# Kernel tuning notes

Hardware: AMD Instinct MI355X
Metric: run time of the kernel (lower is better)

Reference implementation:

```python
import jax, jax.numpy as jnp
import numpy as np

BN_EPS = 1e-5


def setup_inputs() -> dict:
    key = jax.random.key(0)
    ks = jax.random.split(key, 12)
    B, N, S, D1, D2 = 8, 8192, 2048, 128, 256
    C_in = D2 + D1  # 384
    mlp = [256, 128]
    inp = {
        "xyz1": jax.random.normal(ks[0], (B, 3, N), jnp.float32),
        "xyz2": jax.random.normal(ks[1], (B, 3, S), jnp.float32),
        "points1": jax.random.normal(ks[2], (B, D1, N), jnp.float32),
        "points2": jax.random.normal(ks[3], (B, D2, S), jnp.float32),
    }
    # conv0: in 384 -> 256, conv1: 256 -> 128 (1x1 Conv1d == per-point matmul)
    inp["w0"] = jax.random.normal(ks[4], (mlp[0], C_in), jnp.float32) * (1.0 / np.sqrt(C_in))
    inp["b0"] = jax.random.normal(ks[5], (mlp[0],), jnp.float32) * 0.01
    inp["g0"] = jnp.ones((mlp[0],), jnp.float32)
    inp["be0"] = jnp.zeros((mlp[0],), jnp.float32)
    inp["w1"] = jax.random.normal(ks[6], (mlp[1], mlp[0]), jnp.float32) * (1.0 / np.sqrt(mlp[0]))
    inp["b1"] = jax.random.normal(ks[7], (mlp[1],), jnp.float32) * 0.01
    inp["g1"] = jnp.ones((mlp[1],), jnp.float32)
    inp["be1"] = jnp.zeros((mlp[1],), jnp.float32)
    return inp


def _conv_bn_relu(x, w, b, g, be):
    # 1x1 Conv1d + BatchNorm1d (training-mode batch stats, biased var) + ReLU
    x = jnp.einsum("oc,bcn->bon", w, x) + b[None, :, None]
    m = jnp.mean(x, axis=(0, 2), keepdims=True)
    v = jnp.var(x, axis=(0, 2), keepdims=True)
    x = (x - m) * jax.lax.rsqrt(v + BN_EPS) * g[None, :, None] + be[None, :, None]
    return jax.nn.relu(x)


def reference(xyz1, xyz2, points1, points2, w0, b0, g0, be0, w1, b1, g1, be1):
    B, _, N = xyz1.shape
    S = xyz2.shape[2]
    src = jnp.transpose(xyz1, (0, 2, 1))  # [B,N,3]
    dst = jnp.transpose(xyz2, (0, 2, 1))  # [B,S,3]
    # squared pairwise distance [B,N,S]
    dist = (
        jnp.sum(src * src, axis=-1)[:, :, None]
        + jnp.sum(dst * dst, axis=-1)[:, None, :]
        - 2.0 * jnp.einsum("bnc,bsc->bns", src, dst)
    )
    # 3 nearest neighbors (smallest dist, sorted)
    neg_d, idx = jax.lax.top_k(-dist, 3)  # [B,N,3]
    d3 = -neg_d
    recip = 1.0 / (d3 + 1e-8)
    weight = recip / jnp.sum(recip, axis=-1, keepdims=True)  # [B,N,3]
    p2t = jnp.transpose(points2, (0, 2, 1))  # [B,S,D']
    gathered = jnp.take_along_axis(
        p2t, idx.reshape(B, N * 3)[:, :, None], axis=1
    ).reshape(B, N, 3, -1)  # [B,N,3,D']
    interp = jnp.einsum("bnkd,bnk->bdn", gathered, weight)  # [B,D',N]
    x = jnp.concatenate([interp, points1], axis=1)  # [B,D'+D,N]
    x = _conv_bn_relu(x, w0, b0, g0, be0)
    x = _conv_bn_relu(x, w1, b1, g1, be1)
    return x
```

## Files before the change

### kernel.cpp

```cpp
#include <hip/hip_runtime.h>
#include <hip/hip_bf16.h>

constexpr int kB = 8, kN = 8192, kS = 2048;
constexpr int kD1 = 128, kD2 = 256, kCin = 384, kM0 = 256, kM1 = 128;
constexpr float kEps = 1e-5f;

typedef float f32x4 __attribute__((ext_vector_type(4)));
typedef short bf16x8 __attribute__((ext_vector_type(8)));
typedef unsigned short u16x4 __attribute__((ext_vector_type(4)));

__device__ inline unsigned short f2bf(float f) {
    __hip_bfloat16 h = __float2bfloat16(f);
    return *reinterpret_cast<unsigned short*>(&h);
}
__device__ inline float bf2f(unsigned short u) {
    unsigned int v = (unsigned int)u << 16;
    return *reinterpret_cast<float*>(&v);
}
__device__ inline unsigned uminu(unsigned a, unsigned b) { return a < b ? a : b; }
__device__ inline unsigned med3u(unsigned a, unsigned b, unsigned c) {
    unsigned d;
    asm("v_med3_u32 %0, %1, %2, %3" : "=v"(d) : "v"(a), "v"(b), "v"(c));
    return d;
}
#define INS4(K0, K1, K2, K3, X) do { unsigned _x = (X);          \
    K3 = med3u(_x, K2, K3);                                      \
    K2 = med3u(_x, K1, K2);                                      \
    K1 = med3u(_x, K0, K1);                                      \
    K0 = uminu(_x, K0); } while (0)

__global__ __launch_bounds__(256) void prep_kernel(
    const float* __restrict__ points2, float* __restrict__ p2t,
    const float* __restrict__ points1, unsigned short* __restrict__ xt,
    const float* __restrict__ xyz2, f32x4* __restrict__ spk, float* __restrict__ stats)
{
    __shared__ float tl[64][69];
    const int bx = blockIdx.x;
    const int t = threadIdx.x;
    const int rlo = t >> 4, rhi = t & 15;
    if (bx < 1024) {
        const int b = bx >> 7, tile = bx & 127;
        const int s0 = (tile & 31) * 64, c0 = (tile >> 5) * 64;
#pragma unroll
        for (int r = 0; r < 4; ++r) {
            const int cl = rlo + r * 16;
            f32x4 v = *(const f32x4*)(points2 + ((size_t)(b * kD2 + c0 + cl)) * kS + s0 + rhi * 4);
#pragma unroll
            for (int j = 0; j < 4; ++j) tl[cl][rhi * 4 + j] = v[j];
        }
        __syncthreads();
#pragma unroll
        for (int r = 0; r < 4; ++r) {
            const int sl = rlo + r * 16;
            f32x4 v;
#pragma unroll
            for (int j = 0; j < 4; ++j) v[j] = tl[rhi * 4 + j][sl];
            *(f32x4*)(p2t + ((size_t)(b * kS + s0 + sl)) * kD2 + c0 + rhi * 4) = v;
        }
    } else if (bx < 3072) {
        const int idx = bx - 1024;
        const int b = idx >> 8, tile = idx & 255;
        const int n0 = (tile & 127) * 64, c0 = (tile >> 7) * 64;
#pragma unroll
        for (int r = 0; r < 4; ++r) {
            const int cl = rlo + r * 16;
            f32x4 v = *(const f32x4*)(points1 + ((size_t)(b * kD1 + c0 + cl)) * kN + n0 + rhi * 4);
#pragma unroll
            for (int j = 0; j < 4; ++j) tl[cl][rhi * 4 + j] = v[j];
        }
        __syncthreads();
#pragma unroll
        for (int r = 0; r < 4; ++r) {
            const int nl = rlo + r * 16;
            u16x4 u;
#pragma unroll
            for (int j = 0; j < 4; ++j) u[j] = f2bf(tl[rhi * 4 + j][nl]);
            *(u16x4*)(xt + ((size_t)(b * kN + n0 + nl)) * kCin + 256 + c0 + rhi * 4) = u;
        }
    } else {
        const int b = bx - 3072;
        const float* x2 = xyz2 + b * 3 * kS;
        for (int s = t; s < kS; s += 256) {
            float sx = x2[s], sy = x2[kS + s], sz = x2[2 * kS + s];
            f32x4 q = {sx, sy, sz, fmaf(sx, sx, fmaf(sy, sy, sz * sz))};
            spk[b * kS + s] = q;
        }
        if (b == 0) for (int i = t; i < 1792; i += 256) stats[i] = 0.f;
    }
}

__global__ __launch_bounds__(256) void knn_interp_kernel(
    const float* __restrict__ xyz1, const f32x4* __restrict__ spk,
    const float* __restrict__ p2t, unsigned short* __restrict__ xt,
    int* __restrict__ flaglist, int* __restrict__ flagcount)
{
    __shared__ f32x4 sp[kS];
    const int bb = blockIdx.x >> 7;
    const int nblk = (blockIdx.x & 127) << 6;
    const int t = threadIdx.x;
    for (int s = t; s < kS; s += 256) sp[s] = spk[bb * kS + s];
    __syncthreads();
    const int q = t >> 2, c = t & 3;
    const int nq = nblk + q;
    const float* x1 = xyz1 + bb * 3 * kN;
    const float px = x1[nq], py = x1[kN + nq], pz = x1[2 * kN + nq];
    const float ax = -2.f * px, ay = -2.f * py, az = -2.f * pz;
    const float pp = fmaf(px, px, fmaf(py, py, pz * pz));

    unsigned k0 = 0xFFFFFFFFu, k1 = 0xFFFFFFFFu, k2 = 0xFFFFFFFFu, k3 = 0xFFFFFFFFu;
#pragma unroll 8
    for (int i = 0; i < 512; ++i) {
        const f32x4 qv = sp[4 * i + c];
        const float e = fmaxf(fmaf(ax, qv[0], fmaf(ay, qv[1], fmaf(az, qv[2], qv[3] + pp))), 0.f);
        const unsigned x = (__float_as_uint(e) & 0xFFFFF800u) | (unsigned)(4 * i + c);
        INS4(k0, k1, k2, k3, x);
    }
#pragma unroll
    for (int off = 1; off <= 2; off <<= 1) {
        const unsigned m0 = __shfl_xor(k0, off), m1 = __shfl_xor(k1, off);
        const unsigned m2 = __shfl_xor(k2, off), m3 = __shfl_xor(k3, off);
        INS4(k0, k1, k2, k3, m0); INS4(k0, k1, k2, k3, m1);
        INS4(k0, k1, k2, k3, m2); INS4(k0, k1, k2, k3, m3);
    }

    bool flag = false;
    float w0f = 0.f, w1f = 0.f, w2f = 0.f;
    int i0 = (int)(k0 & 2047u), i1 = (int)(k1 & 2047u), i2 = (int)(k2 & 2047u);
    if (c == 0) {
        const float v2t = __uint_as_float(k2 & 0xFFFFF800u);
        const float v3t = __uint_as_float(k3 & 0xFFFFF800u);
        flag = (v3t - v2t) <= fmaf(v3t, 1e-3f, 2.5e-4f);
        const double dpx = (double)px, dpy = (double)py, dpz = (double)pz;
        const f32x4 s0 = sp[i0], s1 = sp[i1], s2 = sp[i2];
        double d0 = (dpx - s0[0]) * (dpx - s0[0]) + (dpy - s0[1]) * (dpy - s0[1]) + (dpz - s0[2]) * (dpz - s0[2]);
        double d1 = (dpx - s1[0]) * (dpx - s1[0]) + (dpy - s1[1]) * (dpy - s1[1]) + (dpz - s1[2]) * (dpz - s1[2]);
        double d2 = (dpx - s2[0]) * (dpx - s2[0]) + (dpy - s2[1]) * (dpy - s2[1]) + (dpz - s2[2]) * (dpz - s2[2]);
        if (d1 < d0 || (d1 == d0 && i1 < i0)) { double td = d0; d0 = d1; d1 = td; int ti = i0; i0 = i1; i1 = ti; }
        if (d2 < d1 || (d2 == d1 && i2 < i1)) { double td = d1; d1 = d2; d2 = td; int ti = i1; i1 = i2; i2 = ti; }
        if (d1 < d0 || (d1 == d0 && i1 < i0)) { double td = d0; d0 = d1; d1 = td; int ti = i0; i0 = i1; i1 = ti; }
        const double r0 = 1.0 / (d0 + 1e-8), r1 = 1.0 / (d1 + 1e-8), r2 = 1.0 / (d2 + 1e-8);
        const double rs = 1.0 / (r0 + r1 + r2);
        w0f = (float)(r0 * rs); w1f = (float)(r1 * rs); w2f = (float)(r2 * rs);
    }
    const int src = (t & 63) & ~3;
    w0f = __shfl(w0f, src); w1f = __shfl(w1f, src); w2f = __shfl(w2f, src);
    i0 = __shfl(i0, src); i1 = __shfl(i1, src); i2 = __shfl(i2, src);

    {
        const unsigned long long bal = __ballot(flag);
        if (bal) {
            const int l = t & 63;
            int base = 0;
            if (l == 0) base = atomicAdd(flagcount, __popcll(bal));
            base = __shfl(base, 0);
            if (flag) {
                const int pre = __popcll(bal & ((1ull << l) - 1ull));
                flaglist[base + pre] = (bb << 13) | nq;
            }
        }
    }

    const f32x4* row0 = (const f32x4*)(p2t + ((size_t)(bb * kS) + i0) * kD2);
    const f32x4* row1 = (const f32x4*)(p2t + ((size_t)(bb * kS) + i1) * kD2);
    const f32x4* row2 = (const f32x4*)(p2t + ((size_t)(bb * kS) + i2) * kD2);
    unsigned short* dst = xt + ((size_t)(bb * kN) + nq) * kCin;
#pragma unroll 4
    for (int j = 0; j < 16; ++j) {
        const int ch = c + 4 * j;
        f32x4 v = w0f * row0[ch] + w1f * row1[ch] + w2f * row2[ch];
        u16x4 u = {f2bf(v[0]), f2bf(v[1]), f2bf(v[2]), f2bf(v[3])};
        *(u16x4*)(dst + ch * 4) = u;
    }
}
#undef INS4

__global__ __launch_bounds__(256) void knn_fallback_kernel(
    const float* __restrict__ xyz1, const f32x4* __restrict__ spk,
    const float* __restrict__ p2t, unsigned short* __restrict__ xt,
    const int* __restrict__ flaglist, const int* __restrict__ flagcount)
{
    const int cnt = *flagcount;
    const int t = threadIdx.x;
    const int w = t >> 6, l = t & 63;
    for (int idx = blockIdx.x * 4 + w; idx < cnt; idx += gridDim.x * 4) {
        const int code = flaglist[idx];
        const int b = code >> 13, n = code & 8191;
        const float* x1 = xyz1 + b * 3 * kN;
        const double px = (double)x1[n], py = (double)x1[kN + n], pz = (double)x1[2 * kN + n];
        double d0 = 1e300, d1 = 1e300, d2 = 1e300;
        int i0 = 0, i1 = 0, i2 = 0;
        for (int s = l; s < kS; s += 64) {
            const f32x4 q = spk[b * kS + s];
            const double ex = px - (double)q[0], ey = py - (double)q[1], ez = pz - (double)q[2];
            const double d = ex * ex + ey * ey + ez * ez;
            if (d < d2) {
                if (d < d1) {
                    if (d < d0) { d2 = d1; i2 = i1; d1 = d0; i1 = i0; d0 = d; i0 = s; }
                    else        { d2 = d1; i2 = i1; d1 = d;  i1 = s; }
                } else          { d2 = d;  i2 = s; }
            }
        }
#pragma unroll
        for (int off = 1; off < 64; off <<= 1) {
            double pd0 = __shfl_xor(d0, off), pd1 = __shfl_xor(d1, off), pd2 = __shfl_xor(d2, off);
            int pi0 = __shfl_xor(i0, off), pi1 = __shfl_xor(i1, off), pi2 = __shfl_xor(i2, off);
#pragma unroll
            for (int m = 0; m < 3; ++m) {
                const double pd = (m == 0) ? pd0 : (m == 1) ? pd1 : pd2;
                const int pi = (m == 0) ? pi0 : (m == 1) ? pi1 : pi2;
                if (pd < d2 || (pd == d2 && pi < i2)) {
                    if (pd < d1 || (pd == d1 && pi < i1)) {
                        if (pd < d0 || (pd == d0 && pi < i0)) {
                            d2 = d1; i2 = i1; d1 = d0; i1 = i0; d0 = pd; i0 = pi;
                        } else { d2 = d1; i2 = i1; d1 = pd; i1 = pi; }
                    } else { d2 = pd; i2 = pi; }
                }
            }
        }
        const double r0 = 1.0 / (d0 + 1e-8), r1 = 1.0 / (d1 + 1e-8), r2 = 1.0 / (d2 + 1e-8);
        const double rs = 1.0 / (r0 + r1 + r2);
        const float w0f = (float)(r0 * rs), w1f = (float)(r1 * rs), w2f = (float)(r2 * rs);
        const f32x4* row0 = (const f32x4*)(p2t + ((size_t)(b * kS) + i0) * kD2);
        const f32x4* row1 = (const f32x4*)(p2t + ((size_t)(b * kS) + i1) * kD2);
        const f32x4* row2 = (const f32x4*)(p2t + ((size_t)(b * kS) + i2) * kD2);
        const f32x4 v = w0f * row0[l] + w1f * row1[l] + w2f * row2[l];
        u16x4 u = {f2bf(v[0]), f2bf(v[1]), f2bf(v[2]), f2bf(v[3])};
        *(u16x4*)(xt + ((size_t)(b * kN) + n) * kCin + l * 4) = u;
    }
}

__device__ inline int swz(int row, int ks) {
    return row * 32 + ((ks ^ ((row >> 1) & 3)) << 3);
}

template <int K, int MTOT, bool BNRELU, int OUTMODE, bool STATS>
__global__ __launch_bounds__(256) void gemm_bn_kernel(
    const float* __restrict__ W, const unsigned short* __restrict__ X,
    const float* __restrict__ bn_sum, const float* __restrict__ bn_sq,
    const float* __restrict__ bn_g, const float* __restrict__ bn_be,
    unsigned short* __restrict__ Yb, float* __restrict__ Yf,
    float* __restrict__ gsum, float* __restrict__ gsq)
{
    constexpr int BM = 128, BN = 128;
    __shared__ unsigned short Al[BM * 32], Bl[BN * 32];
    __shared__ float ssum[BM], ssq[BM];
    __shared__ float s_sc[K > 0 ? K : 1], s_sh[K > 0 ? K : 1];
    const int t = threadIdx.x;
    const int bn = blockIdx.x * BN, bo = blockIdx.y * BM, b = blockIdx.z;
    const int l = t & 63, w = t >> 6;
    const int wm = (w >> 1) * 64, wn = (w & 1) * 64;
    const int lrow = l & 15, lks = l >> 4;

    if constexpr (BNRELU) {
        if (t < K) {
            const float invn = 1.0f / 65536.0f;
            const float mean = bn_sum[t] * invn;
            const float var = bn_sq[t] * invn - mean * mean;
            const float sc = bn_g[t] * rsqrtf(var + kEps);
            s_sc[t] = sc;
            s_sh[t] = fmaf(-mean, sc, bn_be[t]);
        }
    }
    if constexpr (STATS) {
        if (t < BM) { ssum[t] = 0.f; ssq[t] = 0.f; }
    }
    __syncthreads();

    f32x4 acc[4][4] = {};
    for (int k0 = 0; k0 < K; k0 += 32) {
#pragma unroll
        for (int r = 0; r < 2; ++r) {
            const int sid = t + r * 256;
            const int m = sid >> 2, ks = sid & 3;
            const float* wp = W + (size_t)(bo + m) * K + k0 + ks * 8;
            f32x4 wa = *(const f32x4*)wp, wb = *(const f32x4*)(wp + 4);
            bf16x8 u;
#pragma unroll
            for (int j = 0; j < 4; ++j) { u[j] = (short)f2bf(wa[j]); u[j + 4] = (short)f2bf(wb[j]); }
            *(bf16x8*)(Al + swz(m, ks)) = u;
        }
#pragma unroll
        for (int r = 0; r < 2; ++r) {
            const int sid = t + r * 256;
            const int nl = sid >> 2, ks = sid & 3;
            bf16x8 v = *(const bf16x8*)(X + ((size_t)(b * kN) + bn + nl) * K + k0 + ks * 8);
            if constexpr (BNRELU) {
#pragma unroll
                for (int j = 0; j < 8; ++j) {
                    const int ch = k0 + ks * 8 + j;
                    float f = fmaxf(fmaf(bf2f((unsigned short)v[j]), s_sc[ch], s_sh[ch]), 0.f);
                    v[j] = (short)f2bf(f);
                }
            }
            *(bf16x8*)(Bl + swz(nl, ks)) = v;
        }
        __syncthreads();
        bf16x8 af[4], bfr[4];
#pragma unroll
        for (int f = 0; f < 4; ++f) af[f]  = *(const bf16x8*)(Al + swz(wm + f * 16 + lrow, lks));
#pragma unroll
        for (int f = 0; f < 4; ++f) bfr[f] = *(const bf16x8*)(Bl + swz(wn + f * 16 + lrow, lks));
#pragma unroll
        for (int mi = 0; mi < 4; ++mi)
#pragma unroll
            for (int ni = 0; ni < 4; ++ni)
                acc[mi][ni] = __builtin_amdgcn_mfma_f32_16x16x32_bf16(af[mi], bfr[ni], acc[mi][ni], 0, 0, 0);
        __syncthreads();
    }

    if constexpr (STATS) {
#pragma unroll
        for (int mi = 0; mi < 4; ++mi) {
#pragma unroll
            for (int r = 0; r < 4; ++r) {
                float ps = 0.f, pq = 0.f;
#pragma unroll
                for (int ni = 0; ni < 4; ++ni) { float v = acc[mi][ni][r]; ps += v; pq += v * v; }
#pragma unroll
                for (int off = 1; off < 16; off <<= 1) { ps += __shfl_xor(ps, off); pq += __shfl_xor(pq, off); }
                if (lrow == 0) {
                    const int m = wm + mi * 16 + lks * 4 + r;
                    atomicAdd(&ssum[m], ps); atomicAdd(&ssq[m], pq);
                }
            }
        }
    }

    if constexpr (OUTMODE == 0) {
#pragma unroll
        for (int mi = 0; mi < 4; ++mi)
#pragma unroll
            for (int ni = 0; ni < 4; ++ni) {
                const int m = bo + wm + mi * 16 + lks * 4;
                const int n = bn + wn + ni * 16 + lrow;
                u16x4 u = {f2bf(acc[mi][ni][0]), f2bf(acc[mi][ni][1]),
                           f2bf(acc[mi][ni][2]), f2bf(acc[mi][ni][3])};
                *(u16x4*)(Yb + ((size_t)(b * kN) + n) * MTOT + m) = u;
            }
    } else {
#pragma unroll
        for (int mi = 0; mi < 4; ++mi)
#pragma unroll
            for (int ni = 0; ni < 4; ++ni) {
                const int n = bn + wn + ni * 16 + lrow;
#pragma unroll
                for (int r = 0; r < 4; ++r) {
                    const int m = bo + wm + mi * 16 + lks * 4 + r;
                    Yf[((size_t)(b * MTOT) + m) * kN + n] = acc[mi][ni][r];
                }
            }
    }
    if constexpr (STATS) {
        __syncthreads();
        if (t < BM) {
            atomicAdd(&gsum[bo + t], ssum[t]);
            atomicAdd(&gsq[bo + t], ssq[t]);
        }
    }
}

__global__ __launch_bounds__(256) void bn_relu_out_kernel(
    float* __restrict__ out, const float* __restrict__ bn_sum, const float* __restrict__ bn_sq,
    const float* __restrict__ bn_g, const float* __restrict__ bn_be)
{
    __shared__ float ssc[kM1], ssh[kM1];
    const int t = threadIdx.x;
    if (t < kM1) {
        const float invn = 1.0f / 65536.0f;
        const float mean = bn_sum[t] * invn;
        const float var = bn_sq[t] * invn - mean * mean;
        const float sc = bn_g[t] * rsqrtf(var + kEps);
        ssc[t] = sc;
        ssh[t] = fmaf(-mean, sc, bn_be[t]);
    }
    __syncthreads();
    const int total = kB * kM1 * kN / 4;
    for (int idx = blockIdx.x * blockDim.x + t; idx < total; idx += gridDim.x * blockDim.x) {
        const int p = (idx >> 11) & 127;
        const float sc = ssc[p], sh = ssh[p];
        f32x4 v = ((f32x4*)out)[idx];
#pragma unroll
        for (int j = 0; j < 4; ++j) v[j] = fmaxf(fmaf(v[j], sc, sh), 0.f);
        ((f32x4*)out)[idx] = v;
    }
}

extern "C" void kernel_launch(void* const* d_in, const int* in_sizes, int n_in,
                              void* d_out, int out_size, void* d_ws, size_t ws_size,
                              hipStream_t stream)
{
    const float* xyz1    = (const float*)d_in[0];
    const float* xyz2    = (const float*)d_in[1];
    const float* points1 = (const float*)d_in[2];
    const float* points2 = (const float*)d_in[3];
    const float* w0      = (const float*)d_in[4];
    const float* g0      = (const float*)d_in[6];
    const float* be0     = (const float*)d_in[7];
    const float* w1      = (const float*)d_in[8];
    const float* g1      = (const float*)d_in[10];
    const float* be1     = (const float*)d_in[11];
    float* out = (float*)d_out;

    char* ws = (char*)d_ws;
    unsigned short* xt  = (unsigned short*)ws;
    float* p2t          = (float*)(ws + (size_t)50331648);
    unsigned short* y0t = (unsigned short*)(ws + (size_t)67108864);
    float* stats        = (float*)(ws + (size_t)100663296);
    f32x4* spk          = (f32x4*)(ws + (size_t)104857600);
    int*  flaglist      = (int*)(ws + (size_t)105906176);
    float* sum0 = stats,          *sq0 = stats + 256;
    float* sum1 = stats + 512,    *sq1 = stats + 640;
    int*  flagcount = (int*)(stats + 1536);

    prep_kernel<<<3080, 256, 0, stream>>>(points2, p2t, points1, xt, xyz2, spk, stats);
    knn_interp_kernel<<<1024, 256, 0, stream>>>(xyz1, spk, p2t, xt, flaglist, flagcount);
    knn_fallback_kernel<<<1024, 256, 0, stream>>>(xyz1, spk, p2t, xt, flaglist, flagcount);
    gemm_bn_kernel<kCin, kM0, false, 0, true><<<dim3(64, 2, 8), 256, 0, stream>>>(
        w0, xt, nullptr, nullptr, nullptr, nullptr, y0t, nullptr, sum0, sq0);
    gemm_bn_kernel<kM0, kM1, true, 1, true><<<dim3(64, 1, 8), 256, 0, stream>>>(
        w1, y0t, sum0, sq0, g0, be0, nullptr, out, sum1, sq1);
    bn_relu_out_kernel<<<2048, 256, 0, stream>>>(out, sum1, sq1, g1, be1);
}
```

Before: 167.9 us.

## Pre-convert weights to bf16, double-buffer GEMM LDS tiles, halve N tile

Weights w0/w1 are now converted to bf16 once inside the prep kernel, so each GEMM block no longer re-reads and re-converts fp32 weights every K step. The GEMM kernel gets register-staged double buffering in LDS: the next tile's global loads are issued before the current tile's MFMAs, and one sync per K step is dropped. The N tile shrinks from 128 to 64, which doubles the grid for better occupancy and load balance but lowers per-block reuse of the A tile. It also adds extra workspace buffers and a few more prep blocks.

```diff
diff --git a/kernel.cpp b/kernel.cpp
--- a/kernel.cpp
+++ b/kernel.cpp
@@ -32,7 +32,9 @@
 __global__ __launch_bounds__(256) void prep_kernel(
     const float* __restrict__ points2, float* __restrict__ p2t,
     const float* __restrict__ points1, unsigned short* __restrict__ xt,
-    const float* __restrict__ xyz2, f32x4* __restrict__ spk, float* __restrict__ stats)
+    const float* __restrict__ xyz2, f32x4* __restrict__ spk, float* __restrict__ stats,
+    const float* __restrict__ w0, unsigned short* __restrict__ w0bf,
+    const float* __restrict__ w1, unsigned short* __restrict__ w1bf)
 {
     __shared__ float tl[64][69];
     const int bx = blockIdx.x;
@@ -77,7 +79,7 @@
             for (int j = 0; j < 4; ++j) u[j] = f2bf(tl[rhi * 4 + j][nl]);
             *(u16x4*)(xt + ((size_t)(b * kN + n0 + nl)) * kCin + 256 + c0 + rhi * 4) = u;
         }
-    } else {
+    } else if (bx < 3080) {
         const int b = bx - 3072;
         const float* x2 = xyz2 + b * 3 * kS;
         for (int s = t; s < kS; s += 256) {
@@ -86,6 +88,20 @@
             spk[b * kS + s] = q;
         }
         if (b == 0) for (int i = t; i < 1792; i += 256) stats[i] = 0.f;
+    } else if (bx < 3096) {
+        const int base = (bx - 3080) * 256 + t;
+        for (int c = base; c < kM0 * kCin / 4; c += 4096) {
+            f32x4 v = *(const f32x4*)(w0 + (size_t)c * 4);
+            u16x4 u = {f2bf(v[0]), f2bf(v[1]), f2bf(v[2]), f2bf(v[3])};
+            *(u16x4*)(w0bf + (size_t)c * 4) = u;
+        }
+    } else {
+        const int base = (bx - 3096) * 256 + t;
+        for (int c = base; c < kM1 * kM0 / 4; c += 2048) {
+            f32x4 v = *(const f32x4*)(w1 + (size_t)c * 4);
+            u16x4 u = {f2bf(v[0]), f2bf(v[1]), f2bf(v[2]), f2bf(v[3])};
+            *(u16x4*)(w1bf + (size_t)c * 4) = u;
+        }
     }
 }
 
@@ -235,20 +251,20 @@
 
 template <int K, int MTOT, bool BNRELU, int OUTMODE, bool STATS>
 __global__ __launch_bounds__(256) void gemm_bn_kernel(
-    const float* __restrict__ W, const unsigned short* __restrict__ X,
+    const unsigned short* __restrict__ Wbf, const unsigned short* __restrict__ X,
     const float* __restrict__ bn_sum, const float* __restrict__ bn_sq,
     const float* __restrict__ bn_g, const float* __restrict__ bn_be,
     unsigned short* __restrict__ Yb, float* __restrict__ Yf,
     float* __restrict__ gsum, float* __restrict__ gsq)
 {
-    constexpr int BM = 128, BN = 128;
-    __shared__ unsigned short Al[BM * 32], Bl[BN * 32];
+    constexpr int BM = 128, BN = 64;
+    __shared__ unsigned short Al[2][BM * 32], Bl[2][BN * 32];
     __shared__ float ssum[BM], ssq[BM];
-    __shared__ float s_sc[K > 0 ? K : 1], s_sh[K > 0 ? K : 1];
+    __shared__ float s_sc[K], s_sh[K];
     const int t = threadIdx.x;
     const int bn = blockIdx.x * BN, bo = blockIdx.y * BM, b = blockIdx.z;
     const int l = t & 63, w = t >> 6;
-    const int wm = (w >> 1) * 64, wn = (w & 1) * 64;
+    const int wm = (w >> 1) * 64, wn = (w & 1) * 32;
     const int lrow = l & 15, lks = l >> 4;
 
     if constexpr (BNRELU) {
@@ -266,45 +282,49 @@
     }
     __syncthreads();
 
-    f32x4 acc[4][4] = {};
-    for (int k0 = 0; k0 < K; k0 += 32) {
-#pragma unroll
-        for (int r = 0; r < 2; ++r) {
-            const int sid = t + r * 256;
-            const int m = sid >> 2, ks = sid & 3;
-            const float* wp = W + (size_t)(bo + m) * K + k0 + ks * 8;
-            f32x4 wa = *(const f32x4*)wp, wb = *(const f32x4*)(wp + 4);
-            bf16x8 u;
-#pragma unroll
-            for (int j = 0; j < 4; ++j) { u[j] = (short)f2bf(wa[j]); u[j + 4] = (short)f2bf(wb[j]); }
-            *(bf16x8*)(Al + swz(m, ks)) = u;
-        }
-#pragma unroll
-        for (int r = 0; r < 2; ++r) {
-            const int sid = t + r * 256;
-            const int nl = sid >> 2, ks = sid & 3;
-            bf16x8 v = *(const bf16x8*)(X + ((size_t)(b * kN) + bn + nl) * K + k0 + ks * 8);
-            if constexpr (BNRELU) {
-#pragma unroll
-                for (int j = 0; j < 8; ++j) {
-                    const int ch = k0 + ks * 8 + j;
-                    float f = fmaxf(fmaf(bf2f((unsigned short)v[j]), s_sc[ch], s_sh[ch]), 0.f);
-                    v[j] = (short)f2bf(f);
-                }
-            }
-            *(bf16x8*)(Bl + swz(nl, ks)) = v;
-        }
-        __syncthreads();
-        bf16x8 af[4], bfr[4];
-#pragma unroll
-        for (int f = 0; f < 4; ++f) af[f]  = *(const bf16x8*)(Al + swz(wm + f * 16 + lrow, lks));
-#pragma unroll
-        for (int f = 0; f < 4; ++f) bfr[f] = *(const bf16x8*)(Bl + swz(wn + f * 16 + lrow, lks));
+    const int mA0 = t >> 2, ksA = t & 3;
+    const int mA1 = mA0 + 64;
+    const int nB = t >> 2, ksB = t & 3;
+    bf16x8 rA0, rA1, rB;
+
+    auto load_tile = [&](int k0) {
+        rA0 = *(const bf16x8*)(Wbf + (size_t)(bo + mA0) * K + k0 + ksA * 8);
+        rA1 = *(const bf16x8*)(Wbf + (size_t)(bo + mA1) * K + k0 + ksA * 8);
+        rB  = *(const bf16x8*)(X + ((size_t)(b * kN) + bn + nB) * K + k0 + ksB * 8);
+    };
+    auto write_tile = [&](int buf, int k0) {
+        *(bf16x8*)(&Al[buf][0] + swz(mA0, ksA)) = rA0;
+        *(bf16x8*)(&Al[buf][0] + swz(mA1, ksA)) = rA1;
+        bf16x8 v = rB;
+        if constexpr (BNRELU) {
+#pragma unroll
+            for (int j = 0; j < 8; ++j) {
+                const int ch = k0 + ksB * 8 + j;
+                float f = fmaxf(fmaf(bf2f((unsigned short)v[j]), s_sc[ch], s_sh[ch]), 0.f);
+                v[j] = (short)f2bf(f);
+            }
+        }
+        *(bf16x8*)(&Bl[buf][0] + swz(nB, ksB)) = v;
+    };
+
+    f32x4 acc[4][2] = {};
+    load_tile(0);
+    write_tile(0, 0);
+    __syncthreads();
+    int cur = 0;
+    for (int k0 = 32; k0 <= K; k0 += 32) {
+        if (k0 < K) load_tile(k0);
+        bf16x8 af[4], bfr[2];
+#pragma unroll
+        for (int f = 0; f < 4; ++f) af[f]  = *(const bf16x8*)(&Al[cur][0] + swz(wm + f * 16 + lrow, lks));
+#pragma unroll
+        for (int f = 0; f < 2; ++f) bfr[f] = *(const bf16x8*)(&Bl[cur][0] + swz(wn + f * 16 + lrow, lks));
 #pragma unroll
         for (int mi = 0; mi < 4; ++mi)
 #pragma unroll
-            for (int ni = 0; ni < 4; ++ni)
+            for (int ni = 0; ni < 2; ++ni)
                 acc[mi][ni] = __builtin_amdgcn_mfma_f32_16x16x32_bf16(af[mi], bfr[ni], acc[mi][ni], 0, 0, 0);
+        if (k0 < K) { write_tile(cur ^ 1, k0); cur ^= 1; }
         __syncthreads();
     }
 
@@ -315,7 +335,7 @@
             for (int r = 0; r < 4; ++r) {
                 float ps = 0.f, pq = 0.f;
 #pragma unroll
-                for (int ni = 0; ni < 4; ++ni) { float v = acc[mi][ni][r]; ps += v; pq += v * v; }
+                for (int ni = 0; ni < 2; ++ni) { float v = acc[mi][ni][r]; ps += v; pq += v * v; }
 #pragma unroll
                 for (int off = 1; off < 16; off <<= 1) { ps += __shfl_xor(ps, off); pq += __shfl_xor(pq, off); }
                 if (lrow == 0) {
@@ -330,7 +350,7 @@
 #pragma unroll
         for (int mi = 0; mi < 4; ++mi)
 #pragma unroll
-            for (int ni = 0; ni < 4; ++ni) {
+            for (int ni = 0; ni < 2; ++ni) {
                 const int m = bo + wm + mi * 16 + lks * 4;
                 const int n = bn + wn + ni * 16 + lrow;
                 u16x4 u = {f2bf(acc[mi][ni][0]), f2bf(acc[mi][ni][1]),
@@ -341,7 +361,7 @@
 #pragma unroll
         for (int mi = 0; mi < 4; ++mi)
 #pragma unroll
-            for (int ni = 0; ni < 4; ++ni) {
+            for (int ni = 0; ni < 2; ++ni) {
                 const int n = bn + wn + ni * 16 + lrow;
 #pragma unroll
                 for (int r = 0; r < 4; ++r) {
@@ -408,16 +428,19 @@
     float* stats        = (float*)(ws + (size_t)100663296);
     f32x4* spk          = (f32x4*)(ws + (size_t)104857600);
     int*  flaglist      = (int*)(ws + (size_t)105906176);
+    unsigned short* w0bf = (unsigned short*)(ws + (size_t)106954752);
+    unsigned short* w1bf = (unsigned short*)(ws + (size_t)107151360);
     float* sum0 = stats,          *sq0 = stats + 256;
     float* sum1 = stats + 512,    *sq1 = stats + 640;
     int*  flagcount = (int*)(stats + 1536);
 
-    prep_kernel<<<3080, 256, 0, stream>>>(points2, p2t, points1, xt, xyz2, spk, stats);
+    prep_kernel<<<3104, 256, 0, stream>>>(points2, p2t, points1, xt, xyz2, spk, stats,
+                                          w0, w0bf, w1, w1bf);
     knn_interp_kernel<<<1024, 256, 0, stream>>>(xyz1, spk, p2t, xt, flaglist, flagcount);
     knn_fallback_kernel<<<1024, 256, 0, stream>>>(xyz1, spk, p2t, xt, flaglist, flagcount);
-    gemm_bn_kernel<kCin, kM0, false, 0, true><<<dim3(64, 2, 8), 256, 0, stream>>>(
-        w0, xt, nullptr, nullptr, nullptr, nullptr, y0t, nullptr, sum0, sq0);
-    gemm_bn_kernel<kM0, kM1, true, 1, true><<<dim3(64, 1, 8), 256, 0, stream>>>(
-        w1, y0t, sum0, sq0, g0, be0, nullptr, out, sum1, sq1);
+    gemm_bn_kernel<kCin, kM0, false, 0, true><<<dim3(128, 2, 8), 256, 0, stream>>>(
+        w0bf, xt, nullptr, nullptr, nullptr, nullptr, y0t, nullptr, sum0, sq0);
+    gemm_bn_kernel<kM0, kM1, true, 1, true><<<dim3(128, 1, 8), 256, 0, stream>>>(
+        w1bf, y0t, sum0, sq0, g0, be0, nullptr, out, sum1, sq1);
     bn_relu_out_kernel<<<2048, 256, 0, stream>>>(out, sum1, sq1, g1, be1);
 }
```

Result: slower. 182.8 us (+8.9%).
